# Kernel optimization log

Hardware: AMD Instinct MI355X
Metric: run time of the kernel (lower is better)

Reference implementation:

```python
import jax, jax.numpy as jnp
import numpy as np

# Config matching init_kwargs: N=4 networks, dims 128 -> 1024 -> 1024 -> 512
A, B, D = 8, 2048, 128     # agents, batch, input size
N = 4                       # number of independent SePS networks
H1, H2, H3 = 1024, 1024, 512


def setup_inputs() -> dict:
    key = jax.random.key(0)
    ks = jax.random.split(key, 6)
    inputs = jax.random.normal(ks[0], (A, B, D), dtype=jnp.float32)  # stacked per-agent obs
    seps_indices = jax.random.randint(ks[1], (B, A), 0, N)           # cluster id per (sample, agent)
    scale = lambda k, shape, fan: jax.random.normal(k, shape, dtype=jnp.float32) * (1.0 / np.sqrt(fan))
    W0 = scale(ks[2], (N, D, H1), D);   b0 = jnp.zeros((N, H1), jnp.float32)
    W1 = scale(ks[3], (N, H1, H2), H1); b1 = jnp.zeros((N, H2), jnp.float32)
    W2 = scale(ks[4], (N, H2, H3), H2); b2 = jnp.zeros((N, H3), jnp.float32)
    return {"inputs": inputs, "seps_indices": seps_indices,
            "W0": W0, "b0": b0, "W1": W1, "b1": b1, "W2": W2, "b2": b2}


def reference(inputs, seps_indices, W0, b0, W1, b1, W2, b2):
    # Run every network densely on the full stacked input, as the torch module does.
    # inputs: [A, B, D]; W*: [N, in, out]
    h = jax.nn.relu(jnp.einsum('abd,ndh->nabh', inputs, W0) + b0[:, None, None, :])
    h = jax.nn.relu(jnp.einsum('nabh,nhk->nabk', h, W1) + b1[:, None, None, :])
    out_all = jnp.einsum('nabk,nko->nabo', h, W2) + b2[:, None, None, :]  # [N, A, B, H3]
    # Gather along the network axis per (agent, sample): seps_indices is [B, A]
    idx = seps_indices.T                              # [A, B]
    a = jnp.arange(inputs.shape[0])[:, None]          # [A, 1]
    b = jnp.arange(inputs.shape[1])[None, :]          # [1, B]
    return out_all[idx, a, b, :]                      # [A, B, H3] (stacked per-agent outputs)
```

## Files before the change

kernel.cpp:

```cpp
#include <hip/hip_runtime.h>
#include <hip/hip_bf16.h>

#define AG 8
#define BT 2048
#define RT (AG*BT)
#define NNET 4
#define D0 128
#define H1 1024
#define H2 1024
#define H3 512

typedef __attribute__((ext_vector_type(8))) short short8;
typedef __attribute__((ext_vector_type(4))) float f32x4;

__device__ __forceinline__ float bf2f(unsigned short u){
  return __uint_as_float(((unsigned int)u) << 16);
}
__device__ __forceinline__ unsigned short f2bf(float f){
  unsigned int x = __float_as_uint(f);
  x += 0x7fff + ((x >> 16) & 1);
  return (unsigned short)(x >> 16);
}

__device__ __forceinline__ void gload_lds16(const void* g, void* l){
  __builtin_amdgcn_global_load_lds(
      (const __attribute__((address_space(1))) unsigned int*)g,
      (__attribute__((address_space(3))) unsigned int*)l, 16, 0, 0);
}

__device__ __forceinline__ int bucket_off(const int* counts, int n){
  int s = 0;
  #pragma unroll
  for (int i = 0; i < NNET-1; i++) if (i < n) s += counts[i];
  return s;
}

__global__ void k_init(int* counts){
  if (threadIdx.x < NNET) counts[threadIdx.x] = 0;
}

__global__ __launch_bounds__(256) void k_compact(const int* __restrict__ seps,
                          int* __restrict__ counts, int* __restrict__ rowlist){
  __shared__ int lcount[NNET];
  __shared__ int lbase[NNET];
  int t = blockIdx.x * 256 + threadIdx.x;
  if (threadIdx.x < NNET) lcount[threadIdx.x] = 0;
  __syncthreads();
  int a = t >> 11, b = t & (BT-1);
  int n = seps[b*AG + a];
  int lrank = atomicAdd(&lcount[n], 1);
  __syncthreads();
  if (threadIdx.x < NNET)
    lbase[threadIdx.x] = atomicAdd(&counts[threadIdx.x], lcount[threadIdx.x]);
  __syncthreads();
  rowlist[n*RT + lbase[n] + lrank] = t;
}

template<int K, int NOUT>
__global__ __launch_bounds__(256) void k_transpose(const float* __restrict__ W,
                                                   unsigned short* __restrict__ WT){
  __shared__ float tile[32][33];
  int n = blockIdx.z;
  int k0 = blockIdx.x*32, o0 = blockIdx.y*32;
  const float* Wn = W + (size_t)n*K*NOUT;
  unsigned short* WTn = WT + (size_t)n*NOUT*K;
  int tx = threadIdx.x & 31, ty0 = threadIdx.x >> 5;
  #pragma unroll
  for (int r = 0; r < 32; r += 8)
    tile[ty0 + r][tx] = Wn[(size_t)(k0 + ty0 + r)*NOUT + o0 + tx];
  __syncthreads();
  #pragma unroll
  for (int r = 0; r < 32; r += 8)
    WTn[(size_t)(o0 + ty0 + r)*K + k0 + tx] = f2bf(tile[tx][ty0 + r]);
}

__global__ __launch_bounds__(256) void k_gather0(const float* __restrict__ X,
                          const int* __restrict__ counts,
                          const int* __restrict__ rowlist, unsigned short* __restrict__ X0h){
  int n = blockIdx.y;
  int cnt = counts[n];
  int i = blockIdx.x*16 + (threadIdx.x >> 4);
  if (i >= cnt) return;
  int off = bucket_off(counts, n);
  int orig = rowlist[n*RT + i];
  int c = (threadIdx.x & 15) * 8;
  const float* src = X + (size_t)orig*D0 + c;
  float4 v0 = *(const float4*)src, v1 = *(const float4*)(src+4);
  ushort4 u0, u1;
  u0.x=f2bf(v0.x); u0.y=f2bf(v0.y); u0.z=f2bf(v0.z); u0.w=f2bf(v0.w);
  u1.x=f2bf(v1.x); u1.y=f2bf(v1.y); u1.z=f2bf(v1.z); u1.w=f2bf(v1.w);
  unsigned short* dst = X0h + (size_t)(off + i)*D0 + c;
  *(ushort4*)dst = u0; *(ushort4*)(dst+4) = u1;
}

template<int K, int NOUT, int RELU, int SCATTER>
__global__ __launch_bounds__(256) void k_mlp(
    const unsigned short* __restrict__ X,
    const unsigned short* __restrict__ WT,
    const float* __restrict__ Bias,
    const int* __restrict__ counts,
    const int* __restrict__ rowlist,
    unsigned short* __restrict__ Yh,
    float* __restrict__ Yf)
{
  const int n = blockIdx.z;
  const int cnt = counts[n];
  const int i0 = blockIdx.x * 128;
  if (i0 >= cnt) return;
  const int off = bucket_off(counts, n);
  const int bn = blockIdx.y * 128;

  __shared__ __align__(16) unsigned short As[128*32];
  __shared__ __align__(16) unsigned short Bs[128*32];
  __shared__ int rs[128];

  const int t = threadIdx.x, lane = t & 63, wave = t >> 6;
  const int wm = wave >> 1, wn = wave & 1;
  const int lr = lane & 15, g = lane >> 4;

  if (SCATTER && t < 128) rs[t] = rowlist[n*RT + min(i0 + t, cnt-1)];

  const unsigned short* pA[2]; const unsigned short* pB[2];
  unsigned int ldsoff[2];
  const unsigned short* WTn = WT + (size_t)n * NOUT * K;
  #pragma unroll
  for (int j = 0; j < 2; j++){
    int r  = (j*4 + wave)*16 + (lane >> 2);
    int ps = lane & 3;
    int ls = ps ^ ((r >> 1) & 3);
    int rA = min(i0 + r, cnt-1);
    pA[j] = X   + (size_t)(off + rA)*K + ls*8;
    pB[j] = WTn + (size_t)(bn  + r )*K + ls*8;
    ldsoff[j] = (unsigned)(j*4 + wave) * 512;
  }

  int aoff[4], boff[4];
  #pragma unroll
  for (int i = 0; i < 4; i++){
    int ra = wm*64 + i*16 + lr;
    aoff[i] = ra*32 + (g ^ ((ra>>1)&3))*8;
    int rb = wn*64 + i*16 + lr;
    boff[i] = rb*32 + (g ^ ((rb>>1)&3))*8;
  }

  f32x4 acc[4][4] = {};
  for (int k0 = 0; k0 < K; k0 += 32){
    #pragma unroll
    for (int j = 0; j < 2; j++){
      gload_lds16(pA[j], &As[ldsoff[j]]);
      gload_lds16(pB[j], &Bs[ldsoff[j]]);
      pA[j] += 32; pB[j] += 32;
    }
    __syncthreads();

    short8 av[4], bv[4];
    #pragma unroll
    for (int i = 0; i < 4; i++) av[i] = *(const short8*)&As[aoff[i]];
    #pragma unroll
    for (int i = 0; i < 4; i++) bv[i] = *(const short8*)&Bs[boff[i]];
    #pragma unroll
    for (int mi = 0; mi < 4; mi++)
      #pragma unroll
      for (int ni = 0; ni < 4; ni++)
        acc[mi][ni] = __builtin_amdgcn_mfma_f32_16x16x32_bf16(av[mi], bv[ni], acc[mi][ni], 0, 0, 0);
    __syncthreads();
  }

  float bias4[4];
  #pragma unroll
  for (int ni = 0; ni < 4; ni++)
    bias4[ni] = Bias[n*NOUT + bn + wn*64 + ni*16 + lr];

  #pragma unroll
  for (int mi = 0; mi < 4; mi++){
    #pragma unroll
    for (int i = 0; i < 4; i++){
      int rloc = wm*64 + mi*16 + g*4 + i;
      int grow = i0 + rloc;
      if (grow < cnt){
        #pragma unroll
        for (int ni = 0; ni < 4; ni++){
          float v = acc[mi][ni][i] + bias4[ni];
          if (RELU) v = fmaxf(v, 0.f);
          int col = bn + wn*64 + ni*16 + lr;
          if (SCATTER) Yf[(size_t)rs[rloc]*NOUT + col] = v;
          else         Yh[(size_t)(off + grow)*NOUT + col] = f2bf(v);
        }
      }
    }
  }
}

extern "C" void kernel_launch(void* const* d_in, const int* in_sizes, int n_in,
                              void* d_out, int out_size, void* d_ws, size_t ws_size,
                              hipStream_t stream) {
  const float* inputs = (const float*)d_in[0];
  const int*   seps   = (const int*)  d_in[1];
  const float* W0     = (const float*)d_in[2];
  const float* b0     = (const float*)d_in[3];
  const float* W1     = (const float*)d_in[4];
  const float* b1     = (const float*)d_in[5];
  const float* W2     = (const float*)d_in[6];
  const float* b2     = (const float*)d_in[7];
  float* out = (float*)d_out;

  char* ws = (char*)d_ws;
  int* counts  = (int*)ws;
  int* rowlist = (int*)(ws + 4096);
  const size_t MB = 1u << 20;
  unsigned short* WT0 = (unsigned short*)(ws + 1*MB);
  unsigned short* WT1 = (unsigned short*)(ws + 2*MB);
  unsigned short* WT2 = (unsigned short*)(ws + 10*MB);
  unsigned short* h1  = (unsigned short*)(ws + 14*MB);
  unsigned short* h2  = (unsigned short*)(ws + 46*MB);
  unsigned short* X0h = (unsigned short*)(ws + 46*MB);

  k_init   <<<1, 64, 0, stream>>>(counts);
  k_compact<<<RT/256, 256, 0, stream>>>(seps, counts, rowlist);

  k_transpose<D0, H1><<<dim3(D0/32, H1/32, NNET), 256, 0, stream>>>(W0, WT0);
  k_transpose<H1, H2><<<dim3(H1/32, H2/32, NNET), 256, 0, stream>>>(W1, WT1);
  k_transpose<H2, H3><<<dim3(H2/32, H3/32, NNET), 256, 0, stream>>>(W2, WT2);
  k_gather0<<<dim3(RT/16, NNET), 256, 0, stream>>>(inputs, counts, rowlist, X0h);

  k_mlp<D0, H1, 1, 0><<<dim3(RT/128, H1/128, NNET), 256, 0, stream>>>(
      X0h, WT0, b0, counts, rowlist, h1, nullptr);
  k_mlp<H1, H2, 1, 0><<<dim3(RT/128, H2/128, NNET), 256, 0, stream>>>(
      h1, WT1, b1, counts, rowlist, h2, nullptr);
  k_mlp<H2, H3, 0, 1><<<dim3(RT/128, H3/128, NNET), 256, 0, stream>>>(
      h2, WT2, b2, counts, rowlist, nullptr, out);
}
```

Baseline: 152.2 us.

## Double-buffer LDS tiles in MLP GEMM and vectorize epilogue stores

Adds a two-stage LDS ping-pong so the next K-slice is loaded asynchronously while MFMAs consume the current one, which drops one barrier per iteration. It also swaps the MFMA operands so each lane holds four consecutive output columns, allowing float4/ushort4 stores and vector bias loads in the epilogue. MFMA sections are wrapped in s_setprio. The cost is doubled LDS per block, which may reduce occupancy.

```diff
diff --git a/kernel.cpp b/kernel.cpp
--- a/kernel.cpp
+++ b/kernel.cpp
@@ -110,8 +110,8 @@
   const int off = bucket_off(counts, n);
   const int bn = blockIdx.y * 128;
 
-  __shared__ __align__(16) unsigned short As[128*32];
-  __shared__ __align__(16) unsigned short Bs[128*32];
+  __shared__ __align__(16) unsigned short As[2][128*32];
+  __shared__ __align__(16) unsigned short Bs[2][128*32];
   __shared__ int rs[128];
 
   const int t = threadIdx.x, lane = t & 63, wave = t >> 6;
@@ -143,48 +143,67 @@
     boff[i] = rb*32 + (g ^ ((rb>>1)&3))*8;
   }
 
+  #pragma unroll
+  for (int j = 0; j < 2; j++){
+    gload_lds16(pA[j], &As[0][ldsoff[j]]);
+    gload_lds16(pB[j], &Bs[0][ldsoff[j]]);
+    pA[j] += 32; pB[j] += 32;
+  }
+  __syncthreads();
+
   f32x4 acc[4][4] = {};
+  int cur = 0;
   for (int k0 = 0; k0 < K; k0 += 32){
-    #pragma unroll
-    for (int j = 0; j < 2; j++){
-      gload_lds16(pA[j], &As[ldsoff[j]]);
-      gload_lds16(pB[j], &Bs[ldsoff[j]]);
-      pA[j] += 32; pB[j] += 32;
+    if (k0 + 32 < K){
+      #pragma unroll
+      for (int j = 0; j < 2; j++){
+        gload_lds16(pA[j], &As[cur^1][ldsoff[j]]);
+        gload_lds16(pB[j], &Bs[cur^1][ldsoff[j]]);
+        pA[j] += 32; pB[j] += 32;
+      }
     }
-    __syncthreads();
-
     short8 av[4], bv[4];
     #pragma unroll
-    for (int i = 0; i < 4; i++) av[i] = *(const short8*)&As[aoff[i]];
+    for (int i = 0; i < 4; i++) av[i] = *(const short8*)&As[cur][aoff[i]];
     #pragma unroll
-    for (int i = 0; i < 4; i++) bv[i] = *(const short8*)&Bs[boff[i]];
+    for (int i = 0; i < 4; i++) bv[i] = *(const short8*)&Bs[cur][boff[i]];
+    __builtin_amdgcn_s_setprio(1);
     #pragma unroll
     for (int mi = 0; mi < 4; mi++)
       #pragma unroll
       for (int ni = 0; ni < 4; ni++)
-        acc[mi][ni] = __builtin_amdgcn_mfma_f32_16x16x32_bf16(av[mi], bv[ni], acc[mi][ni], 0, 0, 0);
+        acc[mi][ni] = __builtin_amdgcn_mfma_f32_16x16x32_bf16(bv[ni], av[mi], acc[mi][ni], 0, 0, 0);
+    __builtin_amdgcn_s_setprio(0);
     __syncthreads();
-  }
-
-  float bias4[4];
+    cur ^= 1;
+  }
+
+  f32x4 bias4[4];
   #pragma unroll
   for (int ni = 0; ni < 4; ni++)
-    bias4[ni] = Bias[n*NOUT + bn + wn*64 + ni*16 + lr];
+    bias4[ni] = *(const f32x4*)&Bias[n*NOUT + bn + wn*64 + ni*16 + g*4];
 
   #pragma unroll
   for (int mi = 0; mi < 4; mi++){
-    #pragma unroll
-    for (int i = 0; i < 4; i++){
-      int rloc = wm*64 + mi*16 + g*4 + i;
-      int grow = i0 + rloc;
-      if (grow < cnt){
+    int rloc = wm*64 + mi*16 + lr;
+    int grow = i0 + rloc;
+    if (grow < cnt){
+      #pragma unroll
+      for (int ni = 0; ni < 4; ni++){
+        float o[4];
         #pragma unroll
-        for (int ni = 0; ni < 4; ni++){
-          float v = acc[mi][ni][i] + bias4[ni];
+        for (int i = 0; i < 4; i++){
+          float v = acc[mi][ni][i] + bias4[ni][i];
           if (RELU) v = fmaxf(v, 0.f);
-          int col = bn + wn*64 + ni*16 + lr;
-          if (SCATTER) Yf[(size_t)rs[rloc]*NOUT + col] = v;
-          else         Yh[(size_t)(off + grow)*NOUT + col] = f2bf(v);
+          o[i] = v;
+        }
+        int cb = bn + wn*64 + ni*16 + (g<<2);
+        if (SCATTER){
+          *(float4*)&Yf[(size_t)rs[rloc]*NOUT + cb] = make_float4(o[0],o[1],o[2],o[3]);
+        } else {
+          ushort4 u;
+          u.x=f2bf(o[0]); u.y=f2bf(o[1]); u.z=f2bf(o[2]); u.w=f2bf(o[3]);
+          *(ushort4*)&Yh[(size_t)(off + grow)*NOUT + cb] = u;
         }
       }
     }
```

After: 158.2 us. 1.04x slower.
